# Kernel optimization log

Measured on AMD Instinct MI355X. Metric: run time of the kernel, lower is better.

Reference implementation:

```python
import jax, jax.numpy as jnp
import numpy as np

B, N, DIM_IN, DIM_INNER, DIM_OUT, WINDOW = 4, 4096, 1024, 1024, 1024, 128


def setup_inputs() -> dict:
    key = jax.random.key(0)
    k1, k2, k3, k4 = jax.random.split(key, 4)
    x = jax.random.normal(k1, (B, N, DIM_IN), dtype=jnp.float32)
    # to_qkv: Linear(dim_in, 3*dim_inner, bias=False); stored as [in, 3*inner] for x @ W
    w_qkv = jax.random.normal(k2, (DIM_IN, 3 * DIM_INNER), dtype=jnp.float32) / np.sqrt(DIM_IN)
    # to_out: Linear(dim_inner, dim_out) with bias
    w_out = jax.random.normal(k3, (DIM_INNER, DIM_OUT), dtype=jnp.float32) / np.sqrt(DIM_INNER)
    b_out = jax.random.normal(k4, (DIM_OUT,), dtype=jnp.float32) * 0.01
    return {"x": x, "w_qkv": w_qkv, "w_out": w_out, "b_out": b_out}


def reference(x, w_qkv, w_out, b_out):
    b, n, _ = x.shape
    w = WINDOW
    scale = DIM_INNER ** (-0.5)
    # n is a multiple of window, so pad_to_multiple is a no-op
    qkv = jnp.einsum('bnd,de->bne', x, w_qkv)
    q, k, v = jnp.split(qkv, 3, axis=-1)
    nw = n // w
    win = lambda t: t.reshape(b, nw, w, DIM_INNER)  # b (w n) d -> b w n d
    q, k, v = win(q), win(k), win(v)
    # pad one zero block at the front of the window axis
    kp = jnp.pad(k, ((0, 0), (1, 0), (0, 0), (0, 0)))
    # concat previous block + current block along token axis -> (b, nw, 2w, d)
    k2 = jnp.concatenate([kp[:, :-1], kp[:, 1:]], axis=2)
    # NOTE: faithful to source bug: the lambda references k (not t), so v is
    # overwritten with the concatenated k blocks as well.
    v2 = k2
    sim = jnp.einsum('bwid,bwjd->bwij', q, k2) * scale  # (b, nw, w, 2w)
    i, j = w, 2 * w
    mask = jnp.triu(jnp.ones((i, j), dtype=bool), j - i + 1)  # causal within lookback window
    mask_value = -jnp.finfo(sim.dtype).max
    sim = jnp.where(mask[None, None], mask_value, sim)
    attn = jax.nn.softmax(sim, axis=-1)
    out = jnp.einsum('bwij,bwjd->bwid', attn, v2)
    out = out.reshape(b, n, DIM_INNER)[:, :n]
    return jnp.einsum('bnd,de->bne', out, w_out) + b_out
```

## Files before the change

kernel.cpp:

```cpp
#include <hip/hip_runtime.h>
#include <float.h>


#define B_SZ 4
#define SEQ 4096
#define DIM 1024
#define WIN 128
#define NWIN 32
#define TW 256
#define NROWS (B_SZ * SEQ)
#define KPAD 4224

typedef float f32x4 __attribute__((ext_vector_type(4)));
typedef __bf16 bf16x8 __attribute__((ext_vector_type(8)));

__device__ __forceinline__ unsigned short f2b(float f) {
    unsigned int u = __float_as_uint(f);
    u += 0x7FFF + ((u >> 16) & 1);
    return (unsigned short)(u >> 16);
}

__device__ __forceinline__ void gld_lds16(const unsigned short* g, unsigned short* l) {
    __builtin_amdgcn_global_load_lds(
        (const __attribute__((address_space(1))) void*)g,
        (__attribute__((address_space(3))) void*)l, 16, 0, 0);
}

__device__ __forceinline__ bf16x8 lds_read_swz(const unsigned short* tb, int row, int kbyte) {
    int L = row * 128 + kbyte;
    L ^= ((L >> 9) & 1) << 5;
    return *(const bf16x8*)((const char*)tb + L);
}

#define BAR __builtin_amdgcn_s_barrier()
#define PRI1 __builtin_amdgcn_s_setprio(1)
#define PRI0 __builtin_amdgcn_s_setprio(0)
#define LGKM0 do { asm volatile("s_waitcnt lgkmcnt(0)" ::: "memory"); \
                   __builtin_amdgcn_sched_barrier(0); } while (0)
#define VMW(N) do { asm volatile("s_waitcnt vmcnt(" #N ")" ::: "memory"); \
                    __builtin_amdgcn_sched_barrier(0); } while (0)

#define LDAF(BUF, MH)                                                        \
    _Pragma("unroll") for (int m_ = 0; m_ < 4; ++m_)                         \
    _Pragma("unroll") for (int ks_ = 0; ks_ < 2; ++ks_)                      \
        afq[MH][m_][ks_] = lds_read_swz(bufA[BUF],                           \
            wr * 128 + (MH) * 64 + m_ * 16 + fr, ks_ * 64 + kby);

#define LDBF(BUF, NH)                                                        \
    _Pragma("unroll") for (int n_ = 0; n_ < 2; ++n_)                         \
    _Pragma("unroll") for (int ks_ = 0; ks_ < 2; ++ks_)                      \
        bfq[n_][ks_] = lds_read_swz(bufB[BUF],                               \
            wc * 64 + (NH) * 32 + n_ * 16 + fr, ks_ * 64 + kby);

#define MFQ(MH, NH)                                                          \
    _Pragma("unroll") for (int ks_ = 0; ks_ < 2; ++ks_)                      \
    _Pragma("unroll") for (int m_ = 0; m_ < 4; ++m_)                         \
    _Pragma("unroll") for (int n_ = 0; n_ < 2; ++n_)                         \
        acc[(MH) * 4 + m_][(NH) * 2 + n_] =                                  \
            __builtin_amdgcn_mfma_f32_16x16x32_bf16(afq[MH][m_][ks_],        \
                bfq[n_][ks_], acc[(MH) * 4 + m_][(NH) * 2 + n_], 0, 0, 0);

#define STG_HA(BUF, HALF, K0)                                                \
    { gld_lds16(A + soffA[(HALF) * 2 + 0] + (K0), bufA[BUF] + ldst[(HALF) * 2 + 0]); \
      gld_lds16(A + soffA[(HALF) * 2 + 1] + (K0), bufA[BUF] + ldst[(HALF) * 2 + 1]); }
#define STG_HB(BUF, HALF, K0)                                                \
    { gld_lds16(Bt + soffB[(HALF) * 2 + 0] + (K0), bufB[BUF] + ldst[(HALF) * 2 + 0]); \
      gld_lds16(Bt + soffB[(HALF) * 2 + 1] + (K0), bufB[BUF] + ldst[(HALF) * 2 + 1]); }

__device__ __forceinline__ void core256(
    const unsigned short* __restrict__ A, int lda,
    const unsigned short* __restrict__ Bt, int ldb, int K,
    unsigned short* lds, f32x4 (&acc)[8][4],
    int wid, int lane, int wr, int wc)
{
    unsigned short* bufA[2] = { lds, lds + 32768 };
    unsigned short* bufB[2] = { lds + 16384, lds + 49152 };

    const int kby = (lane >> 4) * 16;
    const int fr = lane & 15;

    int soffA[4], soffB[4], ldst[4];
#pragma unroll
    for (int hj = 0; hj < 4; ++hj) {
        const int half = hj >> 1, j = hj & 1;
        const int P = half * 16384 + wid * 2048 + j * 1024 + lane * 16;
        const int L = P ^ (((P >> 9) & 1) << 5);
        const int row = L >> 7, col = (L & 127) >> 1;
        soffA[hj] = row * lda + col;
        soffB[hj] = row * ldb + col;
        ldst[hj] = (half * 16384 + wid * 2048 + j * 1024) >> 1;
    }

    bf16x8 afq[2][4][2], bfq[2][2];
#pragma unroll
    for (int m = 0; m < 8; ++m)
#pragma unroll
        for (int n = 0; n < 4; ++n) acc[m][n] = (f32x4){0.f, 0.f, 0.f, 0.f};

    STG_HA(0, 0, 0); STG_HA(0, 1, 0); STG_HB(0, 0, 0); STG_HB(0, 1, 0);
    STG_HA(1, 0, 64); STG_HA(1, 1, 64); STG_HB(1, 0, 64);
    VMW(6);
    BAR;

    const int NITER = K >> 7;
#pragma unroll 1
    for (int i = 0; i < NITER; ++i) {
        const bool st = (i + 1 < NITER);
        const int ku1 = (2 * i + 1) * 64;
        const int ku2 = (2 * i + 2) * 64;
        const int ku3 = (2 * i + 3) * 64;

        LDAF(0, 0); LDBF(0, 0);
        STG_HB(1, 1, ku1);
        BAR; LGKM0; PRI1; MFQ(0, 0); PRI0; BAR;
        LDAF(0, 1);
        BAR; LGKM0; PRI1; MFQ(1, 0); PRI0; BAR;
        LDBF(0, 1);
        if (st) STG_HA(0, 0, ku2);
        BAR; LGKM0; PRI1; MFQ(1, 1); PRI0; BAR;
        if (st) { STG_HA(0, 1, ku2); VMW(4); } else { VMW(0); }
        BAR; PRI1; MFQ(0, 1); PRI0; BAR;
        LDAF(1, 0); LDBF(1, 0);
        if (st) STG_HB(0, 0, ku2);
        BAR; LGKM0; PRI1; MFQ(0, 0); PRI0; BAR;
        LDAF(1, 1);
        if (st) STG_HB(0, 1, ku2);
        BAR; LGKM0; PRI1; MFQ(1, 0); PRI0; BAR;
        LDBF(1, 1);
        if (st) STG_HA(1, 0, ku3);
        BAR; LGKM0; PRI1; MFQ(1, 1); PRI0; BAR;
        if (st) { STG_HA(1, 1, ku3); STG_HB(1, 0, ku3); VMW(6); } else { VMW(0); }
        BAR; PRI1; MFQ(0, 1); PRI0; BAR;
    }
}

__device__ __forceinline__ void mfma_core(
    const unsigned short* __restrict__ A, int lda,
    const unsigned short* __restrict__ Bt, int ldb, int K,
    unsigned short* As, unsigned short* Bs, f32x4 (&acc)[4][4])
{
    const int tid = threadIdx.x;
    const int wv = tid >> 6, lane = tid & 63;
    const int wr = wv >> 1, wc = wv & 1;

#pragma unroll
    for (int m = 0; m < 4; ++m)
#pragma unroll
        for (int n = 0; n < 4; ++n) acc[m][n] = (f32x4){0.f, 0.f, 0.f, 0.f};

    for (int k0 = 0; k0 < K; k0 += 64) {
#pragma unroll
        for (int it = 0; it < 4; ++it) {
            int rbase = wv * 32 + it * 8;
            const unsigned short* g =
                A + (size_t)(rbase + (lane >> 3)) * lda + k0 + (lane & 7) * 8;
            gld_lds16(g, As + rbase * 64);
        }
#pragma unroll
        for (int it = 0; it < 4; ++it) {
            int rbase = wv * 32 + it * 8;
            const unsigned short* g =
                Bt + (size_t)(rbase + (lane >> 3)) * ldb + k0 + (lane & 7) * 8;
            gld_lds16(g, Bs + rbase * 64);
        }
        __syncthreads();

#pragma unroll
        for (int ks = 0; ks < 2; ++ks) {
            bf16x8 af[4], bfr[4];
            const int kof = ks * 32 + (lane >> 4) * 8;
#pragma unroll
            for (int m = 0; m < 4; ++m)
                af[m] = *(const bf16x8*)(As + (wr * 64 + m * 16 + (lane & 15)) * 64 + kof);
#pragma unroll
            for (int n = 0; n < 4; ++n)
                bfr[n] = *(const bf16x8*)(Bs + (wc * 64 + n * 16 + (lane & 15)) * 64 + kof);
#pragma unroll
            for (int m = 0; m < 4; ++m)
#pragma unroll
                for (int n = 0; n < 4; ++n)
                    acc[m][n] = __builtin_amdgcn_mfma_f32_16x16x32_bf16(
                        af[m], bfr[n], acc[m][n], 0, 0, 0);
        }
        __syncthreads();
    }
}

__global__ __launch_bounds__(256) void k_prep_x(const float* __restrict__ x,
                                                unsigned short* __restrict__ xb)
{
    int i = blockIdx.x * 256 + threadIdx.x;
    float4 a = *(const float4*)&x[(size_t)i * 8];
    float4 b = *(const float4*)&x[(size_t)i * 8 + 4];
    ushort4 lo, hi;
    lo.x = f2b(a.x); lo.y = f2b(a.y); lo.z = f2b(a.z); lo.w = f2b(a.w);
    hi.x = f2b(b.x); hi.y = f2b(b.y); hi.z = f2b(b.z); hi.w = f2b(b.w);
    *(ushort4*)&xb[(size_t)i * 8] = lo;
    *(ushort4*)&xb[(size_t)i * 8 + 4] = hi;
}

__global__ __launch_bounds__(256) void k_transpose(const float* __restrict__ src,
    int src_ld, int col0, int R, unsigned short* __restrict__ dst)
{
    __shared__ float T[32][33];
    const int r0 = blockIdx.y * 32, c0 = blockIdx.x * 32;
    const int cx = threadIdx.x & 31, ry = threadIdx.x >> 5;
#pragma unroll
    for (int i = 0; i < 4; ++i)
        T[ry + 8 * i][cx] = src[(size_t)(r0 + ry + 8 * i) * src_ld + col0 + c0 + cx];
    __syncthreads();
#pragma unroll
    for (int i = 0; i < 4; ++i)
        dst[(size_t)(c0 + ry + 8 * i) * R + r0 + cx] = f2b(T[cx][ry + 8 * i]);
}

__global__ __launch_bounds__(256) void k_zero_kpad(unsigned short* __restrict__ kbuf)
{
    int t = blockIdx.x * 256 + threadIdx.x;
    int b = t >> 14, r = t & 16383;
    float4 z = {0.f, 0.f, 0.f, 0.f};
    *(float4*)&kbuf[(size_t)b * KPAD * DIM + (size_t)r * 8] = z;
}

__global__ __launch_bounds__(256) void k_zero_ktpad(unsigned short* __restrict__ ktr)
{
    int t = blockIdx.x * 256 + threadIdx.x;
    int b = t >> 14, rem = t & 16383;
    int d = rem >> 4, s = rem & 15;
    float4 z = {0.f, 0.f, 0.f, 0.f};
    *(float4*)&ktr[((size_t)b * DIM + d) * KPAD + s * 8] = z;
}

__global__ __launch_bounds__(512, 2) void k_gemm_qk(
    const unsigned short* __restrict__ xb, const unsigned short* __restrict__ wqkvT,
    unsigned short* __restrict__ qbuf, unsigned short* __restrict__ kbuf,
    unsigned short* __restrict__ ktr)
{
    __shared__ unsigned short lds[65536];
    const int tid = threadIdx.x, wid = tid >> 6, lane = tid & 63;
    const int wr = wid >> 2, wc = wid & 3;
    const int wg = blockIdx.x;
    const int x = (wg & 7) * 64 + (wg >> 3);
    const int bm = (x & 63) * 256;
    const int bn = (x >> 6) * 256;

    f32x4 acc[8][4];
    core256(xb + (size_t)bm * DIM, DIM, wqkvT + (size_t)bn * DIM, DIM, DIM,
            lds, acc, wid, lane, wr, wc);

    const int fr = lane & 15;
#pragma unroll
    for (int m = 0; m < 8; ++m) {
        const int row0 = bm + wr * 128 + m * 16 + (lane >> 4) * 4;
#pragma unroll
        for (int n = 0; n < 4; ++n) {
            const int col = bn + wc * 64 + n * 16 + fr;
            if (col < DIM) {
#pragma unroll
                for (int r = 0; r < 4; ++r)
                    qbuf[(size_t)(row0 + r) * DIM + col] = f2b(acc[m][n][r]);
            } else {
                const int d = col - DIM;
                const int b = row0 >> 12, tok0 = row0 & 4095;
#pragma unroll
                for (int r = 0; r < 4; ++r)
                    kbuf[((size_t)b * KPAD + 128 + tok0 + r) * DIM + d] = f2b(acc[m][n][r]);
                ushort4 kt;
                kt.x = f2b(acc[m][n][0]); kt.y = f2b(acc[m][n][1]);
                kt.z = f2b(acc[m][n][2]); kt.w = f2b(acc[m][n][3]);
                *(ushort4*)&ktr[((size_t)b * DIM + d) * KPAD + 128 + tok0] = kt;
            }
        }
    }
}

__global__ __launch_bounds__(512, 2) void k_out(
    const unsigned short* __restrict__ aout, const unsigned short* __restrict__ woutT,
    const float* __restrict__ bias, float* __restrict__ out)
{
    __shared__ unsigned short lds[65536];
    const int tid = threadIdx.x, wid = tid >> 6, lane = tid & 63;
    const int wr = wid >> 2, wc = wid & 3;
    const int wg = blockIdx.x;
    const int x = (wg & 7) * 32 + (wg >> 3);
    const int bm = (x & 63) * 256;
    const int bn = (x >> 6) * 256;

    f32x4 acc[8][4];
    core256(aout + (size_t)bm * DIM, DIM, woutT + (size_t)bn * DIM, DIM, DIM,
            lds, acc, wid, lane, wr, wc);

    const int fr = lane & 15;
#pragma unroll
    for (int m = 0; m < 8; ++m) {
        const int row0 = bm + wr * 128 + m * 16 + (lane >> 4) * 4;
#pragma unroll
        for (int n = 0; n < 4; ++n) {
            const int col = bn + wc * 64 + n * 16 + fr;
            const float bb = bias[col];
#pragma unroll
            for (int r = 0; r < 4; ++r)
                out[(size_t)(row0 + r) * DIM + col] = acc[m][n][r] + bb;
        }
    }
}

__global__ __launch_bounds__(256) void k_sim(
    const unsigned short* __restrict__ qbuf, const unsigned short* __restrict__ kbuf,
    float* __restrict__ sim)
{
    __shared__ unsigned short As[128 * 64], Bs[128 * 64];
    f32x4 acc[4][4];
    const int win = blockIdx.y, ct = blockIdx.x;
    const int b = win >> 5, w = win & 31;
    const unsigned short* Ap = qbuf + ((size_t)b * SEQ + w * WIN) * DIM;
    const unsigned short* Bp = kbuf + ((size_t)b * KPAD + w * WIN + ct * 128) * DIM;
    mfma_core(Ap, DIM, Bp, DIM, DIM, As, Bs, acc);

    const int tid = threadIdx.x, wv = tid >> 6, lane = tid & 63;
    const int wr = wv >> 1, wc = wv & 1;
    const float scale = 0.03125f;
#pragma unroll
    for (int m = 0; m < 4; ++m) {
        const int qi0 = wr * 64 + m * 16 + (lane >> 4) * 4;
#pragma unroll
        for (int n = 0; n < 4; ++n) {
            const int jc = ct * 128 + wc * 64 + n * 16 + (lane & 15);
#pragma unroll
            for (int r = 0; r < 4; ++r) {
                const int qi = qi0 + r;
                float v = (jc > qi + WIN) ? -FLT_MAX : acc[m][n][r] * scale;
                sim[((size_t)win * WIN + qi) * TW + jc] = v;
            }
        }
    }
}

__global__ __launch_bounds__(256) void k_softmax(const float* __restrict__ sim,
                                                 unsigned short* __restrict__ attnb)
{
    const int row = blockIdx.x * 4 + (threadIdx.x >> 6);
    const int lane = threadIdx.x & 63;
    const float* p = sim + (size_t)row * TW;
    float4 v = *(const float4*)&p[lane * 4];
    float m = fmaxf(fmaxf(v.x, v.y), fmaxf(v.z, v.w));
#pragma unroll
    for (int off = 32; off; off >>= 1) m = fmaxf(m, __shfl_xor(m, off));
    float e0 = expf(v.x - m), e1 = expf(v.y - m);
    float e2 = expf(v.z - m), e3 = expf(v.w - m);
    float s = e0 + e1 + e2 + e3;
#pragma unroll
    for (int off = 32; off; off >>= 1) s += __shfl_xor(s, off);
    float inv = 1.f / s;
    ushort4 o;
    o.x = f2b(e0 * inv); o.y = f2b(e1 * inv); o.z = f2b(e2 * inv); o.w = f2b(e3 * inv);
    *(ushort4*)&attnb[(size_t)row * TW + lane * 4] = o;
}

__global__ __launch_bounds__(256) void k_pv(
    const unsigned short* __restrict__ attnb, const unsigned short* __restrict__ ktr,
    unsigned short* __restrict__ aout)
{
    __shared__ unsigned short As[128 * 64], Bs[128 * 64];
    f32x4 acc[4][4];
    const int win = blockIdx.y, ct = blockIdx.x;
    const int b = win >> 5, w = win & 31;
    const unsigned short* Ap = attnb + (size_t)win * WIN * TW;
    const unsigned short* Bp = ktr + ((size_t)b * DIM + ct * 128) * KPAD + w * WIN;
    mfma_core(Ap, TW, Bp, KPAD, TW, As, Bs, acc);

    const int tid = threadIdx.x, wv = tid >> 6, lane = tid & 63;
    const int wr = wv >> 1, wc = wv & 1;
#pragma unroll
    for (int m = 0; m < 4; ++m) {
        const int row0 = wr * 64 + m * 16 + (lane >> 4) * 4;
#pragma unroll
        for (int n = 0; n < 4; ++n) {
            const int col = ct * 128 + wc * 64 + n * 16 + (lane & 15);
#pragma unroll
            for (int r = 0; r < 4; ++r)
                aout[((size_t)b * SEQ + w * WIN + row0 + r) * DIM + col] =
                    f2b(acc[m][n][r]);
        }
    }
}

extern "C" void kernel_launch(void* const* d_in, const int* in_sizes, int n_in,
                              void* d_out, int out_size, void* d_ws, size_t ws_size,
                              hipStream_t stream)
{
    const float* x     = (const float*)d_in[0];
    const float* w_qkv = (const float*)d_in[1];
    const float* w_out = (const float*)d_in[2];
    const float* b_out = (const float*)d_in[3];
    float* out = (float*)d_out;

    char* p = (char*)d_ws;
    unsigned short* xb    = (unsigned short*)p; p += (size_t)NROWS * DIM * 2;
    unsigned short* wqkvT = (unsigned short*)p; p += (size_t)2 * DIM * DIM * 2;
    unsigned short* woutT = (unsigned short*)p; p += (size_t)DIM * DIM * 2;
    unsigned short* qbuf  = (unsigned short*)p; p += (size_t)NROWS * DIM * 2;
    unsigned short* kbuf  = (unsigned short*)p; p += (size_t)B_SZ * KPAD * DIM * 2;
    unsigned short* ktr   = (unsigned short*)p; p += (size_t)B_SZ * DIM * KPAD * 2;
    float*          simb  = (float*)p;          p += (size_t)NROWS * TW * 4;
    unsigned short* attnb = (unsigned short*)p; p += (size_t)NROWS * TW * 2;
    unsigned short* aout  = (unsigned short*)p; p += (size_t)NROWS * DIM * 2;

    k_prep_x<<<NROWS * DIM / 8 / 256, 256, 0, stream>>>(x, xb);
    k_transpose<<<dim3(2 * DIM / 32, DIM / 32), 256, 0, stream>>>(w_qkv, 3 * DIM, 0, DIM, wqkvT);
    k_transpose<<<dim3(DIM / 32, DIM / 32), 256, 0, stream>>>(w_out, DIM, 0, DIM, woutT);
    k_zero_kpad<<<256, 256, 0, stream>>>(kbuf);
    k_zero_ktpad<<<256, 256, 0, stream>>>(ktr);

    k_gemm_qk<<<512, 512, 0, stream>>>(xb, wqkvT, qbuf, kbuf, ktr);
    k_sim<<<dim3(2, B_SZ * NWIN), 256, 0, stream>>>(qbuf, kbuf, simb);
    k_softmax<<<NROWS / 4, 256, 0, stream>>>(simb, attnb);
    k_pv<<<dim3(DIM / 128, B_SZ * NWIN), 256, 0, stream>>>(attnb, ktr, aout);
    k_out<<<256, 512, 0, stream>>>(aout, woutT, b_out, out);
}
```

Before: 366.1 us.

## Fuse sim and softmax kernels and drop transposed K buffer

Merges the QK^T score kernel and the softmax kernel into one kernel. Each block computes a 64x256 score tile, reduces row max and row sum across waves through shared memory, and writes bf16 probabilities directly, so the fp32 sim buffer is never written or read back. Separately, it removes the transposed K copy (ktr), its zero-fill kernel and the extra store in the QKV GEMM; the PV kernel instead transposes K tiles into LDS from kbuf. This saves memory traffic and two launches, at the cost of a scalar LDS transpose in PV and a different tile shape for the score GEMM.

Result: no change. 367.7 us (+0.4%).

```diff
diff --git a/kernel.cpp b/kernel.cpp
--- a/kernel.cpp
+++ b/kernel.cpp
@@ -13,6 +13,7 @@
 
 typedef float f32x4 __attribute__((ext_vector_type(4)));
 typedef __bf16 bf16x8 __attribute__((ext_vector_type(8)));
+typedef unsigned short u16x8 __attribute__((ext_vector_type(8)));
 
 __device__ __forceinline__ unsigned short f2b(float f) {
     unsigned int u = __float_as_uint(f);
@@ -134,58 +135,6 @@
     }
 }
 
-__device__ __forceinline__ void mfma_core(
-    const unsigned short* __restrict__ A, int lda,
-    const unsigned short* __restrict__ Bt, int ldb, int K,
-    unsigned short* As, unsigned short* Bs, f32x4 (&acc)[4][4])
-{
-    const int tid = threadIdx.x;
-    const int wv = tid >> 6, lane = tid & 63;
-    const int wr = wv >> 1, wc = wv & 1;
-
-#pragma unroll
-    for (int m = 0; m < 4; ++m)
-#pragma unroll
-        for (int n = 0; n < 4; ++n) acc[m][n] = (f32x4){0.f, 0.f, 0.f, 0.f};
-
-    for (int k0 = 0; k0 < K; k0 += 64) {
-#pragma unroll
-        for (int it = 0; it < 4; ++it) {
-            int rbase = wv * 32 + it * 8;
-            const unsigned short* g =
-                A + (size_t)(rbase + (lane >> 3)) * lda + k0 + (lane & 7) * 8;
-            gld_lds16(g, As + rbase * 64);
-        }
-#pragma unroll
-        for (int it = 0; it < 4; ++it) {
-            int rbase = wv * 32 + it * 8;
-            const unsigned short* g =
-                Bt + (size_t)(rbase + (lane >> 3)) * ldb + k0 + (lane & 7) * 8;
-            gld_lds16(g, Bs + rbase * 64);
-        }
-        __syncthreads();
-
-#pragma unroll
-        for (int ks = 0; ks < 2; ++ks) {
-            bf16x8 af[4], bfr[4];
-            const int kof = ks * 32 + (lane >> 4) * 8;
-#pragma unroll
-            for (int m = 0; m < 4; ++m)
-                af[m] = *(const bf16x8*)(As + (wr * 64 + m * 16 + (lane & 15)) * 64 + kof);
-#pragma unroll
-            for (int n = 0; n < 4; ++n)
-                bfr[n] = *(const bf16x8*)(Bs + (wc * 64 + n * 16 + (lane & 15)) * 64 + kof);
-#pragma unroll
-            for (int m = 0; m < 4; ++m)
-#pragma unroll
-                for (int n = 0; n < 4; ++n)
-                    acc[m][n] = __builtin_amdgcn_mfma_f32_16x16x32_bf16(
-                        af[m], bfr[n], acc[m][n], 0, 0, 0);
-        }
-        __syncthreads();
-    }
-}
-
 __global__ __launch_bounds__(256) void k_prep_x(const float* __restrict__ x,
                                                 unsigned short* __restrict__ xb)
 {
@@ -222,19 +171,9 @@
     *(float4*)&kbuf[(size_t)b * KPAD * DIM + (size_t)r * 8] = z;
 }
 
-__global__ __launch_bounds__(256) void k_zero_ktpad(unsigned short* __restrict__ ktr)
-{
-    int t = blockIdx.x * 256 + threadIdx.x;
-    int b = t >> 14, rem = t & 16383;
-    int d = rem >> 4, s = rem & 15;
-    float4 z = {0.f, 0.f, 0.f, 0.f};
-    *(float4*)&ktr[((size_t)b * DIM + d) * KPAD + s * 8] = z;
-}
-
 __global__ __launch_bounds__(512, 2) void k_gemm_qk(
     const unsigned short* __restrict__ xb, const unsigned short* __restrict__ wqkvT,
-    unsigned short* __restrict__ qbuf, unsigned short* __restrict__ kbuf,
-    unsigned short* __restrict__ ktr)
+    unsigned short* __restrict__ qbuf, unsigned short* __restrict__ kbuf)
 {
     __shared__ unsigned short lds[65536];
     const int tid = threadIdx.x, wid = tid >> 6, lane = tid & 63;
@@ -265,10 +204,6 @@
 #pragma unroll
                 for (int r = 0; r < 4; ++r)
                     kbuf[((size_t)b * KPAD + 128 + tok0 + r) * DIM + d] = f2b(acc[m][n][r]);
-                ushort4 kt;
-                kt.x = f2b(acc[m][n][0]); kt.y = f2b(acc[m][n][1]);
-                kt.z = f2b(acc[m][n][2]); kt.w = f2b(acc[m][n][3]);
-                *(ushort4*)&ktr[((size_t)b * DIM + d) * KPAD + 128 + tok0] = kt;
             }
         }
     }
@@ -305,72 +240,193 @@
     }
 }
 
-__global__ __launch_bounds__(256) void k_sim(
+__global__ __launch_bounds__(512) void k_simsm(
     const unsigned short* __restrict__ qbuf, const unsigned short* __restrict__ kbuf,
-    float* __restrict__ sim)
-{
-    __shared__ unsigned short As[128 * 64], Bs[128 * 64];
-    f32x4 acc[4][4];
+    unsigned short* __restrict__ attnb)
+{
+    __shared__ unsigned short As[64 * 64];
+    __shared__ unsigned short Bs[256 * 64];
+    __shared__ float smax[4][64];
+    __shared__ float ssum[4][64];
+
+    const int mh = blockIdx.x, win = blockIdx.y;
+    const int b = win >> 5, w = win & 31;
+    const int tid = threadIdx.x, wid = tid >> 6, lane = tid & 63;
+    const int wr = wid >> 2, wc = wid & 3;
+    const int hi = lane >> 4, fr = lane & 15;
+
+    const unsigned short* A  = qbuf + (size_t)(b * SEQ + w * WIN + mh * 64) * DIM;
+    const unsigned short* Bt = kbuf + ((size_t)b * KPAD + w * WIN) * DIM;
+
+    f32x4 acc[2][4];
+#pragma unroll
+    for (int m = 0; m < 2; ++m)
+#pragma unroll
+        for (int n = 0; n < 4; ++n) acc[m][n] = (f32x4){0.f, 0.f, 0.f, 0.f};
+
+    for (int k0 = 0; k0 < DIM; k0 += 64) {
+        gld_lds16(A + (size_t)(wid * 8 + (lane >> 3)) * DIM + k0 + (lane & 7) * 8,
+                  As + wid * 512);
+#pragma unroll
+        for (int it = 0; it < 4; ++it)
+            gld_lds16(Bt + (size_t)(it * 64 + wid * 8 + (lane >> 3)) * DIM + k0 + (lane & 7) * 8,
+                      Bs + it * 4096 + wid * 512);
+        __syncthreads();
+#pragma unroll
+        for (int ks = 0; ks < 2; ++ks) {
+            bf16x8 af[2], bf[4];
+            const int kof = ks * 32 + hi * 8;
+#pragma unroll
+            for (int m = 0; m < 2; ++m)
+                af[m] = *(const bf16x8*)(As + (wr * 32 + m * 16 + fr) * 64 + kof);
+#pragma unroll
+            for (int n = 0; n < 4; ++n)
+                bf[n] = *(const bf16x8*)(Bs + (wc * 64 + n * 16 + fr) * 64 + kof);
+#pragma unroll
+            for (int m = 0; m < 2; ++m)
+#pragma unroll
+                for (int n = 0; n < 4; ++n)
+                    acc[m][n] = __builtin_amdgcn_mfma_f32_16x16x32_bf16(
+                        af[m], bf[n], acc[m][n], 0, 0, 0);
+        }
+        __syncthreads();
+    }
+
+    const float scale = 0.03125f;
+    float ms[2][4][4];
+#pragma unroll
+    for (int m = 0; m < 2; ++m)
+#pragma unroll
+        for (int r = 0; r < 4; ++r) {
+            const int qi = mh * 64 + wr * 32 + m * 16 + hi * 4 + r;
+#pragma unroll
+            for (int n = 0; n < 4; ++n) {
+                const int jc = wc * 64 + n * 16 + fr;
+                ms[m][n][r] = (jc > qi + WIN) ? -FLT_MAX : acc[m][n][r] * scale;
+            }
+        }
+
+    float pmv[2][4];
+#pragma unroll
+    for (int m = 0; m < 2; ++m)
+#pragma unroll
+        for (int r = 0; r < 4; ++r) {
+            float pm = fmaxf(fmaxf(ms[m][0][r], ms[m][1][r]),
+                             fmaxf(ms[m][2][r], ms[m][3][r]));
+#pragma unroll
+            for (int off = 1; off < 16; off <<= 1) pm = fmaxf(pm, __shfl_xor(pm, off));
+            pmv[m][r] = pm;
+        }
+    if (fr == 0) {
+#pragma unroll
+        for (int m = 0; m < 2; ++m)
+#pragma unroll
+            for (int r = 0; r < 4; ++r)
+                smax[wc][wr * 32 + m * 16 + hi * 4 + r] = pmv[m][r];
+    }
+    __syncthreads();
+
+    float e[2][4][4], psv[2][4];
+#pragma unroll
+    for (int m = 0; m < 2; ++m)
+#pragma unroll
+        for (int r = 0; r < 4; ++r) {
+            const int rl = wr * 32 + m * 16 + hi * 4 + r;
+            const float rm = fmaxf(fmaxf(smax[0][rl], smax[1][rl]),
+                                   fmaxf(smax[2][rl], smax[3][rl]));
+            float s = 0.f;
+#pragma unroll
+            for (int n = 0; n < 4; ++n) {
+                e[m][n][r] = expf(ms[m][n][r] - rm);
+                s += e[m][n][r];
+            }
+#pragma unroll
+            for (int off = 1; off < 16; off <<= 1) s += __shfl_xor(s, off);
+            psv[m][r] = s;
+        }
+    if (fr == 0) {
+#pragma unroll
+        for (int m = 0; m < 2; ++m)
+#pragma unroll
+            for (int r = 0; r < 4; ++r)
+                ssum[wc][wr * 32 + m * 16 + hi * 4 + r] = psv[m][r];
+    }
+    __syncthreads();
+
+#pragma unroll
+    for (int m = 0; m < 2; ++m)
+#pragma unroll
+        for (int r = 0; r < 4; ++r) {
+            const int rl = wr * 32 + m * 16 + hi * 4 + r;
+            const float inv = 1.f / (ssum[0][rl] + ssum[1][rl] + ssum[2][rl] + ssum[3][rl]);
+            const size_t rowg = (size_t)win * WIN + mh * 64 + rl;
+#pragma unroll
+            for (int n = 0; n < 4; ++n)
+                attnb[rowg * TW + wc * 64 + n * 16 + fr] = f2b(e[m][n][r] * inv);
+        }
+}
+
+__global__ __launch_bounds__(256) void k_pv(
+    const unsigned short* __restrict__ attnb, const unsigned short* __restrict__ kbuf,
+    unsigned short* __restrict__ aout)
+{
+    __shared__ unsigned short As[128 * 64];
+    __shared__ unsigned short Bs[128 * 64];
+
     const int win = blockIdx.y, ct = blockIdx.x;
     const int b = win >> 5, w = win & 31;
-    const unsigned short* Ap = qbuf + ((size_t)b * SEQ + w * WIN) * DIM;
-    const unsigned short* Bp = kbuf + ((size_t)b * KPAD + w * WIN + ct * 128) * DIM;
-    mfma_core(Ap, DIM, Bp, DIM, DIM, As, Bs, acc);
-
     const int tid = threadIdx.x, wv = tid >> 6, lane = tid & 63;
     const int wr = wv >> 1, wc = wv & 1;
-    const float scale = 0.03125f;
-#pragma unroll
-    for (int m = 0; m < 4; ++m) {
-        const int qi0 = wr * 64 + m * 16 + (lane >> 4) * 4;
-#pragma unroll
-        for (int n = 0; n < 4; ++n) {
-            const int jc = ct * 128 + wc * 64 + n * 16 + (lane & 15);
-#pragma unroll
-            for (int r = 0; r < 4; ++r) {
-                const int qi = qi0 + r;
-                float v = (jc > qi + WIN) ? -FLT_MAX : acc[m][n][r] * scale;
-                sim[((size_t)win * WIN + qi) * TW + jc] = v;
-            }
-        }
-    }
-}
-
-__global__ __launch_bounds__(256) void k_softmax(const float* __restrict__ sim,
-                                                 unsigned short* __restrict__ attnb)
-{
-    const int row = blockIdx.x * 4 + (threadIdx.x >> 6);
-    const int lane = threadIdx.x & 63;
-    const float* p = sim + (size_t)row * TW;
-    float4 v = *(const float4*)&p[lane * 4];
-    float m = fmaxf(fmaxf(v.x, v.y), fmaxf(v.z, v.w));
-#pragma unroll
-    for (int off = 32; off; off >>= 1) m = fmaxf(m, __shfl_xor(m, off));
-    float e0 = expf(v.x - m), e1 = expf(v.y - m);
-    float e2 = expf(v.z - m), e3 = expf(v.w - m);
-    float s = e0 + e1 + e2 + e3;
-#pragma unroll
-    for (int off = 32; off; off >>= 1) s += __shfl_xor(s, off);
-    float inv = 1.f / s;
-    ushort4 o;
-    o.x = f2b(e0 * inv); o.y = f2b(e1 * inv); o.z = f2b(e2 * inv); o.w = f2b(e3 * inv);
-    *(ushort4*)&attnb[(size_t)row * TW + lane * 4] = o;
-}
-
-__global__ __launch_bounds__(256) void k_pv(
-    const unsigned short* __restrict__ attnb, const unsigned short* __restrict__ ktr,
-    unsigned short* __restrict__ aout)
-{
-    __shared__ unsigned short As[128 * 64], Bs[128 * 64];
+
+    const unsigned short* Ap = attnb + (size_t)win * WIN * TW;
+    const unsigned short* Kp = kbuf + ((size_t)b * KPAD + w * WIN) * DIM + ct * 128;
+
     f32x4 acc[4][4];
-    const int win = blockIdx.y, ct = blockIdx.x;
-    const int b = win >> 5, w = win & 31;
-    const unsigned short* Ap = attnb + (size_t)win * WIN * TW;
-    const unsigned short* Bp = ktr + ((size_t)b * DIM + ct * 128) * KPAD + w * WIN;
-    mfma_core(Ap, TW, Bp, KPAD, TW, As, Bs, acc);
-
-    const int tid = threadIdx.x, wv = tid >> 6, lane = tid & 63;
-    const int wr = wv >> 1, wc = wv & 1;
+#pragma unroll
+    for (int m = 0; m < 4; ++m)
+#pragma unroll
+        for (int n = 0; n < 4; ++n) acc[m][n] = (f32x4){0.f, 0.f, 0.f, 0.f};
+
+    for (int k0 = 0; k0 < TW; k0 += 64) {
+        u16x8 v[4];
+#pragma unroll
+        for (int it = 0; it < 4; ++it)
+            v[it] = *(const u16x8*)&Kp[(size_t)(k0 + it * 16 + (tid >> 4)) * DIM + (tid & 15) * 8];
+        __syncthreads();
+#pragma unroll
+        for (int it = 0; it < 4; ++it) {
+            const int tok = it * 16 + (tid >> 4);
+            const int d0 = (tid & 15) * 8;
+#pragma unroll
+            for (int ee = 0; ee < 8; ++ee)
+                Bs[(d0 + ee) * 64 + tok] = v[it][ee];
+        }
+#pragma unroll
+        for (int it = 0; it < 4; ++it)
+            gld_lds16(Ap + (size_t)(wv * 32 + it * 8 + (lane >> 3)) * TW + k0 + (lane & 7) * 8,
+                      As + (wv * 32 + it * 8) * 64);
+        __syncthreads();
+
+#pragma unroll
+        for (int ks = 0; ks < 2; ++ks) {
+            bf16x8 af[4], bfr[4];
+            const int kof = ks * 32 + (lane >> 4) * 8;
+#pragma unroll
+            for (int m = 0; m < 4; ++m)
+                af[m] = *(const bf16x8*)(As + (wr * 64 + m * 16 + (lane & 15)) * 64 + kof);
+#pragma unroll
+            for (int n = 0; n < 4; ++n)
+                bfr[n] = *(const bf16x8*)(Bs + (wc * 64 + n * 16 + (lane & 15)) * 64 + kof);
+#pragma unroll
+            for (int m = 0; m < 4; ++m)
+#pragma unroll
+                for (int n = 0; n < 4; ++n)
+                    acc[m][n] = __builtin_amdgcn_mfma_f32_16x16x32_bf16(
+                        af[m], bfr[n], acc[m][n], 0, 0, 0);
+        }
+        __syncthreads();
+    }
+
 #pragma unroll
     for (int m = 0; m < 4; ++m) {
         const int row0 = wr * 64 + m * 16 + (lane >> 4) * 4;
@@ -401,8 +457,6 @@
     unsigned short* woutT = (unsigned short*)p; p += (size_t)DIM * DIM * 2;
     unsigned short* qbuf  = (unsigned short*)p; p += (size_t)NROWS * DIM * 2;
     unsigned short* kbuf  = (unsigned short*)p; p += (size_t)B_SZ * KPAD * DIM * 2;
-    unsigned short* ktr   = (unsigned short*)p; p += (size_t)B_SZ * DIM * KPAD * 2;
-    float*          simb  = (float*)p;          p += (size_t)NROWS * TW * 4;
     unsigned short* attnb = (unsigned short*)p; p += (size_t)NROWS * TW * 2;
     unsigned short* aout  = (unsigned short*)p; p += (size_t)NROWS * DIM * 2;
 
@@ -410,11 +464,9 @@
     k_transpose<<<dim3(2 * DIM / 32, DIM / 32), 256, 0, stream>>>(w_qkv, 3 * DIM, 0, DIM, wqkvT);
     k_transpose<<<dim3(DIM / 32, DIM / 32), 256, 0, stream>>>(w_out, DIM, 0, DIM, woutT);
     k_zero_kpad<<<256, 256, 0, stream>>>(kbuf);
-    k_zero_ktpad<<<256, 256, 0, stream>>>(ktr);
-
-    k_gemm_qk<<<512, 512, 0, stream>>>(xb, wqkvT, qbuf, kbuf, ktr);
-    k_sim<<<dim3(2, B_SZ * NWIN), 256, 0, stream>>>(qbuf, kbuf, simb);
-    k_softmax<<<NROWS / 4, 256, 0, stream>>>(simb, attnb);
-    k_pv<<<dim3(DIM / 128, B_SZ * NWIN), 256, 0, stream>>>(attnb, ktr, aout);
+
+    k_gemm_qk<<<512, 512, 0, stream>>>(xb, wqkvT, qbuf, kbuf);
+    k_simsm<<<dim3(2, B_SZ * NWIN), 512, 0, stream>>>(qbuf, kbuf, attnb);
+    k_pv<<<dim3(DIM / 128, B_SZ * NWIN), 256, 0, stream>>>(attnb, kbuf, aout);
     k_out<<<256, 512, 0, stream>>>(aout, woutT, b_out, out);
 }
```
